# Kernel tuning notes

Measured on AMD Instinct MI355X. Metric: run time of the kernel, lower is better.

The kernel has to match this reference:

```python
import jax, jax.numpy as jnp
import numpy as np
import math

B, S, H, NH = 8, 1024, 768, 12
DH = H // NH  # 64
EPS = 1e-5


def layernorm(x, gamma, beta):
    mu = jnp.mean(x, axis=-1, keepdims=True)
    var = jnp.mean(jnp.square(x - mu), axis=-1, keepdims=True)
    return (x - mu) * jax.lax.rsqrt(var + EPS) * gamma + beta


def setup_inputs() -> dict:
    key = jax.random.key(0)
    ks = jax.random.split(key, 12)
    sc = 1.0 / math.sqrt(H)
    return {
        "x1": jax.random.normal(ks[0], (B, S, H), jnp.float32),
        "weight_mask": jax.random.uniform(ks[1], (B, 1, S, S), jnp.float32),
        "Wq": jax.random.normal(ks[2], (H, H), jnp.float32) * sc,
        "bq": jnp.zeros((H,), jnp.float32),
        "Wk": jax.random.normal(ks[3], (H, H), jnp.float32) * sc,
        "bk": jnp.zeros((H,), jnp.float32),
        "Wv": jax.random.normal(ks[4], (H, H), jnp.float32) * sc,
        "bv": jnp.zeros((H,), jnp.float32),
        "g1": jnp.ones((H,), jnp.float32),
        "be1": jnp.zeros((H,), jnp.float32),
        "g2": jnp.ones((H,), jnp.float32),
        "be2": jnp.zeros((H,), jnp.float32),
        "W1": jax.random.normal(ks[5], (H, 2 * H), jnp.float32) * sc,
        "b1": jnp.zeros((2 * H,), jnp.float32),
        "W2": jax.random.normal(ks[6], (2 * H, H), jnp.float32) * (1.0 / math.sqrt(2 * H)),
        "b2": jnp.zeros((H,), jnp.float32),
    }


def reference(x1, weight_mask, Wq, bq, Wk, bk, Wv, bv, g1, be1, g2, be2, W1, b1, W2, b2):
    # QKV projections [B,S,H]
    q_mixed = x1 @ Wq + bq
    k_mixed = x1 @ Wk + bk
    v_mixed = x1 @ Wv + bv

    def heads(t):  # [B,S,H] -> [B,NH,S,DH]
        return t.reshape(B, S, NH, DH).transpose(0, 2, 1, 3)

    q, k, v = heads(q_mixed), heads(k_mixed), heads(v_mixed)
    scores = jnp.einsum("bhqd,bhkd->bhqk", q, k) / math.sqrt(DH)
    probs = jax.nn.softmax(scores, axis=-1)
    probs = probs * weight_mask  # post-softmax elementwise mask
    ctx = jnp.einsum("bhqk,bhkd->bhqd", probs, v)
    ctx = ctx.transpose(0, 2, 1, 3).reshape(B, S, H)

    # residual uses the mixed query (as in the original code); dropout = eval identity
    x = layernorm(ctx + q_mixed, g1, be1)
    ff = jnp.maximum(x @ W1 + b1, 0.0) @ W2 + b2
    out = layernorm(x + ff, g2, be2)
    return out
```

## Files before the change

kernel.cpp:

```cpp
#include <hip/hip_runtime.h>
#include <math.h>

#define Bsz 8
#define Sq  1024
#define Hd  768
#define NHd 12
#define DHd 64
#define QS  2304

typedef __attribute__((ext_vector_type(8))) short bf16x8;
typedef __attribute__((ext_vector_type(4))) short bf16x4;
typedef __attribute__((ext_vector_type(4))) float f32x4;
typedef __attribute__((ext_vector_type(16))) float f32x16;

__device__ __forceinline__ ushort f2bf(float f) {
    unsigned u = __float_as_uint(f);
    u += 0x7fffu + ((u >> 16) & 1u);
    return (ushort)(u >> 16);
}
__device__ __forceinline__ float bf2f(ushort u) {
    return __uint_as_float(((unsigned)u) << 16);
}
__device__ __forceinline__ void load_lds16(const ushort* g, ushort* l) {
    __builtin_amdgcn_global_load_lds((const __attribute__((address_space(1))) void*)g,
                                     (__attribute__((address_space(3))) void*)l, 16, 0, 0);
}
__device__ __forceinline__ float fexp2(float x) {
#if __has_builtin(__builtin_amdgcn_exp2f)
    return __builtin_amdgcn_exp2f(x);
#else
    return exp2f(x);
#endif
}
__device__ __forceinline__ unsigned pkbf(float a, float b) {
#if __has_builtin(__builtin_amdgcn_perm)
    return __builtin_amdgcn_perm(__float_as_uint(b), __float_as_uint(a), 0x07060302u);
#else
    return (__float_as_uint(a) >> 16) | (__float_as_uint(b) & 0xffff0000u);
#endif
}

__device__ __forceinline__ f32x16 mfma32x8(bf16x4 a, bf16x4 b, f32x16 c) {
#if __has_builtin(__builtin_amdgcn_mfma_f32_32x32x8bf16_1k)
    return __builtin_amdgcn_mfma_f32_32x32x8bf16_1k(a, b, c, 0, 0, 0);
#elif __has_builtin(__builtin_amdgcn_mfma_f32_32x32x8_bf16)
    return __builtin_amdgcn_mfma_f32_32x32x8_bf16(a, b, c, 0, 0, 0);
#else
    bf16x8 a8 = {a[0], a[1], a[2], a[3], 0, 0, 0, 0};
    bf16x8 b8 = {b[0], b[1], b[2], b[3], 0, 0, 0, 0};
    return __builtin_amdgcn_mfma_f32_32x32x16_bf16(a8, b8, c, 0, 0, 0);
#endif
}

#define KSCALE 0.18033688f

__global__ __launch_bounds__(256) void prep(const float* __restrict__ x1,
                                            const float* __restrict__ wmask,
                                            const float* __restrict__ Wq,
                                            const float* __restrict__ Wk,
                                            const float* __restrict__ Wv,
                                            const float* __restrict__ W1,
                                            const float* __restrict__ W2,
                                            const float* __restrict__ bq,
                                            const float* __restrict__ bk,
                                            const float* __restrict__ bv,
                                            ushort* __restrict__ xb,
                                            ushort* __restrict__ maskb,
                                            ushort* __restrict__ WqkvT,
                                            ushort* __restrict__ W1T,
                                            ushort* __restrict__ W2T,
                                            float* __restrict__ qkvbias) {
    const int blk = blockIdx.x;
    const int t   = threadIdx.x;
    __shared__ float tl[32][33];

    if (blk < 4032) {
        const float* in; ushort* out; int Kd, Nd, ntx, tile; float sc;
        if (blk < 1728) {
            const int w = blk / 576; tile = blk % 576;
            in  = (w == 0) ? Wq : (w == 1) ? Wk : Wv;
            out = WqkvT + (size_t)w * 768 * 768;
            Kd = 768; Nd = 768; ntx = 24;
            sc = (w == 1) ? KSCALE : 1.0f;
        } else if (blk < 2880) {
            tile = blk - 1728; in = W1; out = W1T; Kd = 768; Nd = 1536; ntx = 48; sc = 1.0f;
        } else {
            tile = blk - 2880; in = W2; out = W2T; Kd = 1536; Nd = 768; ntx = 24; sc = 1.0f;
        }
        const int n0 = (tile % ntx) * 32, k0 = (tile / ntx) * 32;
        const int tx = t & 31, ty = t >> 5;
#pragma unroll
        for (int i = ty; i < 32; i += 8)
            tl[i][tx] = in[(size_t)(k0 + i) * Nd + n0 + tx] * sc;
        __syncthreads();
#pragma unroll
        for (int i = ty; i < 32; i += 8)
            out[(size_t)(n0 + i) * Kd + k0 + tx] = f2bf(tl[tx][i]);
    } else if (blk < 7616) {
        const int cb = blk - 4032;
        const float4* s4;
        ushort4* d4;
        if (cb < 1536) { s4 = (const float4*)x1    + (size_t)cb * 1024;           d4 = (ushort4*)xb    + (size_t)cb * 1024; }
        else           { s4 = (const float4*)wmask + (size_t)(cb - 1536) * 1024;  d4 = (ushort4*)maskb + (size_t)(cb - 1536) * 1024; }
#pragma unroll
        for (int i = t; i < 1024; i += 256) {
            const float4 f = s4[i];
            ushort4 u;
            u.x = f2bf(f.x); u.y = f2bf(f.y); u.z = f2bf(f.z); u.w = f2bf(f.w);
            d4[i] = u;
        }
    } else {
        for (int i = t; i < 2304; i += 256)
            qkvbias[i] = i < 768 ? bq[i] : (i < 1536 ? bk[i - 768] * KSCALE : bv[i - 1536]);
    }
}

template<int TM, bool RELU, bool OUT_BF16, bool WRITE_VT>
__global__ __launch_bounds__(256) void gemm_mfma(const ushort* __restrict__ A,
                                                 const ushort* __restrict__ BT,
                                                 const float* __restrict__ bias,
                                                 void* __restrict__ Cout,
                                                 ushort* __restrict__ vT,
                                                 int M, int N, int K) {
    const int bm = blockIdx.y * (TM * 32);
    const int bn = blockIdx.x * 128;
    const int t  = threadIdx.x;
    const int wave = t >> 6, lane = t & 63;
    const int l15 = lane & 15, quad = lane >> 4;
    const int wm = (wave >> 1) * (TM * 16), wn = (wave & 1) * 64;

    __shared__ ushort As[TM * 32 * 64];
    __shared__ ushort Bs[128 * 64];

    f32x4 acc[TM][4];
#pragma unroll
    for (int i = 0; i < TM; ++i)
#pragma unroll
        for (int j = 0; j < 4; ++j) acc[i][j] = (f32x4){0, 0, 0, 0};

    const int g_pc = t & 7;

    for (int k0 = 0; k0 < K; k0 += 64) {
#pragma unroll
        for (int it = 0; it < TM; ++it) {
            const int row = (it * 256 + t) >> 3;
            const int cb  = g_pc ^ (row & 7);
            load_lds16(A + (size_t)(bm + row) * K + k0 + cb * 8,
                       As + (size_t)(it * 256 + wave * 64) * 8);
        }
#pragma unroll
        for (int it = 0; it < 4; ++it) {
            const int row = (it * 256 + t) >> 3;
            const int cb  = g_pc ^ (row & 7);
            load_lds16(BT + (size_t)(bn + row) * K + k0 + cb * 8,
                       Bs + (size_t)(it * 256 + wave * 64) * 8);
        }
        __syncthreads();
#pragma unroll
        for (int kk = 0; kk < 64; kk += 32) {
            bf16x8 af[TM], bfr[4];
            const int cbk = (kk >> 3) + quad;
#pragma unroll
            for (int i = 0; i < TM; ++i) {
                const int rowA = wm + i * 16 + l15;
                af[i] = *(const bf16x8*)(As + (size_t)(rowA * 8 + (cbk ^ (rowA & 7))) * 8);
            }
#pragma unroll
            for (int j = 0; j < 4; ++j) {
                const int rowB = wn + j * 16 + l15;
                bfr[j] = *(const bf16x8*)(Bs + (size_t)(rowB * 8 + (cbk ^ (rowB & 7))) * 8);
            }
#pragma unroll
            for (int i = 0; i < TM; ++i)
#pragma unroll
                for (int j = 0; j < 4; ++j)
                    acc[i][j] = __builtin_amdgcn_mfma_f32_16x16x32_bf16(af[i], bfr[j], acc[i][j], 0, 0, 0);
        }
        __syncthreads();
    }

    const bool vblk = WRITE_VT && (bn >= 1536);
#pragma unroll
    for (int i = 0; i < TM; ++i) {
        const int m0 = bm + wm + i * 16 + quad * 4;
#pragma unroll
        for (int j = 0; j < 4; ++j) {
            const int n = bn + wn + j * 16 + l15;
            float v4[4];
#pragma unroll
            for (int r = 0; r < 4; ++r) {
                float v = acc[i][j][r] + bias[n];
                if (RELU) v = fmaxf(v, 0.0f);
                v4[r] = v;
            }
            if (vblk) {
                const int d = n - 1536;
                const int b = m0 >> 10, s = m0 & 1023;
                ushort4 pk;
                pk.x = f2bf(v4[0]); pk.y = f2bf(v4[1]); pk.z = f2bf(v4[2]); pk.w = f2bf(v4[3]);
                *(ushort4*)(vT + ((size_t)(b * NHd + (d >> 6)) * 64 + (d & 63)) * Sq + s) = pk;
            } else {
#pragma unroll
                for (int r = 0; r < 4; ++r) {
                    if (OUT_BF16) ((ushort*)Cout)[(size_t)(m0 + r) * N + n] = f2bf(v4[r]);
                    else          ((float*)Cout)[(size_t)(m0 + r) * N + n] = v4[r];
                }
            }
        }
    }
}

__global__ __launch_bounds__(256, 3) void attn_mfma(const ushort* __restrict__ qkv,
                                                    const ushort* __restrict__ vT,
                                                    const ushort* __restrict__ maskb,
                                                    float* __restrict__ ctx) {
    const int nqt = Sq / 128;
    const int bh  = blockIdx.x / nqt;
    const int qt  = blockIdx.x % nqt;
    const int b   = bh / NHd;
    const int h   = bh % NHd;
    const int t   = threadIdx.x;
    const int wave = t >> 6, lane = t & 63;
    const int l31 = lane & 31, H = lane >> 5;

    __shared__ ushort Ks[2 * 4096];
    __shared__ ushort Vs[2 * 4096];

    const size_t rowbase = (size_t)b * Sq;
    const int q0 = qt * 128 + wave * 32;

    bf16x8 qf[4];
    {
        const ushort* qrow = qkv + (rowbase + q0 + l31) * QS + h * DHd + H * 8;
#pragma unroll
        for (int ds = 0; ds < 4; ++ds) qf[ds] = *(const bf16x8*)(qrow + ds * 16);
    }

    int koff[2][4], voff[2][8];
#pragma unroll
    for (int s = 0; s < 2; ++s) {
#pragma unroll
        for (int ds = 0; ds < 4; ++ds)
            koff[s][ds] = ((s * 32 + l31) * 8 + ((H + 2 * ds) ^ (l31 & 7))) * 8;
#pragma unroll
        for (int ks = 0; ks < 8; ++ks)
            voff[s][ks] = ((s * 32 + l31) * 8 + (ks ^ (l31 & 7))) * 8 + H * 4;
    }

    const int s_pc = t & 7;
    const ushort* kptr[2];
    const ushort* vptr[2];
    int sdst[2];
#pragma unroll
    for (int it = 0; it < 2; ++it) {
        const int row  = (it * 256 + t) >> 3;
        const int gcol = s_pc ^ (row & 7);
        kptr[it] = qkv + (rowbase + row) * QS + Hd + h * DHd + gcol * 8;
        vptr[it] = vT + ((size_t)bh * 64 + row) * Sq + gcol * 8;
        sdst[it] = (it * 256 + t) * 8;
    }
    const ushort* mptr = maskb + ((size_t)b * Sq + q0 + l31) * Sq + H * 4;

#pragma unroll
    for (int it = 0; it < 2; ++it) {
        load_lds16(kptr[it], Ks + sdst[it]);  kptr[it] += 64 * QS;
        load_lds16(vptr[it], Vs + sdst[it]);  vptr[it] += 64;
    }
    __syncthreads();

    f32x16 o0, o1;
#pragma unroll
    for (int r = 0; r < 16; ++r) { o0[r] = 0.0f; o1[r] = 0.0f; }
    float rsum = 0.0f;

    for (int kt = 0; kt < 16; ++kt) {
        const int cur = kt & 1;
        ushort* ksb = Ks + cur * 4096;
        ushort* vsb = Vs + cur * 4096;

        if (kt < 15) {
            ushort* kd = Ks + (cur ^ 1) * 4096;
            ushort* vd = Vs + (cur ^ 1) * 4096;
#pragma unroll
            for (int it = 0; it < 2; ++it) {
                load_lds16(kptr[it], kd + sdst[it]);  kptr[it] += 64 * QS;
                load_lds16(vptr[it], vd + sdst[it]);  vptr[it] += 64;
            }
        }

        ushort4 mv[8];
#pragma unroll
        for (int i = 0; i < 8; ++i) mv[i] = *(const ushort4*)(mptr + i * 8);
        mptr += 64;

        f32x16 s0, s1;
#pragma unroll
        for (int r = 0; r < 16; ++r) { s0[r] = 0.0f; s1[r] = 0.0f; }
#pragma unroll
        for (int ds = 0; ds < 4; ++ds) {
            bf16x8 ka = *(const bf16x8*)(ksb + koff[0][ds]);
            bf16x8 kb = *(const bf16x8*)(ksb + koff[1][ds]);
            s0 = __builtin_amdgcn_mfma_f32_32x32x16_bf16(ka, qf[ds], s0, 0, 0, 0);
            s1 = __builtin_amdgcn_mfma_f32_32x32x16_bf16(kb, qf[ds], s1, 0, 0, 0);
        }

        bf16x4 pf[8];
#pragma unroll
        for (int rr = 0; rr < 4; ++rr) {
            float e0[4], e1[4];
#pragma unroll
            for (int j = 0; j < 4; ++j) {
                e0[j] = fexp2(s0[4 * rr + j]);
                e1[j] = fexp2(s1[4 * rr + j]);
                rsum += e0[j] + e1[j];
            }
            union { uint2 u; bf16x4 v; } p0, p1;
            p0.u.x = pkbf(e0[0] * bf2f(mv[rr].x),     e0[1] * bf2f(mv[rr].y));
            p0.u.y = pkbf(e0[2] * bf2f(mv[rr].z),     e0[3] * bf2f(mv[rr].w));
            p1.u.x = pkbf(e1[0] * bf2f(mv[4 + rr].x), e1[1] * bf2f(mv[4 + rr].y));
            p1.u.y = pkbf(e1[2] * bf2f(mv[4 + rr].z), e1[3] * bf2f(mv[4 + rr].w));
            pf[rr]     = p0.v;
            pf[4 + rr] = p1.v;
        }

#pragma unroll
        for (int ks = 0; ks < 8; ++ks) {
            bf16x4 va = *(const bf16x4*)(vsb + voff[0][ks]);
            bf16x4 vb = *(const bf16x4*)(vsb + voff[1][ks]);
            o0 = mfma32x8(pf[ks], va, o0);
            o1 = mfma32x8(pf[ks], vb, o1);
        }
        __syncthreads();
    }

    rsum += __shfl_xor(rsum, 32);

#pragma unroll
    for (int r = 0; r < 16; ++r) {
        const int ql  = (r & 3) + 8 * (r >> 2) + 4 * H;
        const float inv = 1.0f / __shfl(rsum, ql);
        const size_t row = rowbase + q0 + ql;
        ctx[row * Hd + h * DHd + l31]      = o0[r] * inv;
        ctx[row * Hd + h * DHd + 32 + l31] = o1[r] * inv;
    }
}

template<bool RES_BF16, bool EMIT_BF16, bool EMIT_F32>
__global__ __launch_bounds__(256) void ln_fused(const float* __restrict__ a,
                                                const void* __restrict__ res, int res_stride,
                                                const float* __restrict__ g,
                                                const float* __restrict__ be,
                                                float* __restrict__ outf,
                                                ushort* __restrict__ outb) {
    const int row = blockIdx.x;
    const int t   = threadIdx.x;
    const float* pa = a + (size_t)row * Hd;
    __shared__ float red[4];
    float v[3];
#pragma unroll
    for (int i = 0; i < 3; ++i) {
        const int idx = t + i * 256;
        float rv;
        if (RES_BF16) rv = bf2f(((const ushort*)res)[(size_t)row * res_stride + idx]);
        else          rv = ((const float*)res)[(size_t)row * res_stride + idx];
        v[i] = pa[idx] + rv;
    }

    float s = v[0] + v[1] + v[2];
#pragma unroll
    for (int off = 32; off > 0; off >>= 1) s += __shfl_xor(s, off);
    if ((t & 63) == 0) red[t >> 6] = s;
    __syncthreads();
    const float mu = (red[0] + red[1] + red[2] + red[3]) * (1.0f / Hd);
    __syncthreads();

    float sq = 0.0f;
#pragma unroll
    for (int i = 0; i < 3; ++i) {
        v[i] -= mu;
        sq = fmaf(v[i], v[i], sq);
    }
#pragma unroll
    for (int off = 32; off > 0; off >>= 1) sq += __shfl_xor(sq, off);
    if ((t & 63) == 0) red[t >> 6] = sq;
    __syncthreads();
    const float var = (red[0] + red[1] + red[2] + red[3]) * (1.0f / Hd);
    const float rsq = rsqrtf(var + 1e-5f);
#pragma unroll
    for (int i = 0; i < 3; ++i) {
        const int idx = t + i * 256;
        const float o = v[i] * rsq * g[idx] + be[idx];
        if (EMIT_F32)  outf[(size_t)row * Hd + idx] = o;
        if (EMIT_BF16) outb[(size_t)row * Hd + idx] = f2bf(o);
    }
}

extern "C" void kernel_launch(void* const* d_in, const int* in_sizes, int n_in,
                              void* d_out, int out_size, void* d_ws, size_t ws_size,
                              hipStream_t stream) {
    const float* x1    = (const float*)d_in[0];
    const float* wmask = (const float*)d_in[1];
    const float* Wq    = (const float*)d_in[2];
    const float* bq    = (const float*)d_in[3];
    const float* Wk    = (const float*)d_in[4];
    const float* bk    = (const float*)d_in[5];
    const float* Wv    = (const float*)d_in[6];
    const float* bv    = (const float*)d_in[7];
    const float* g1    = (const float*)d_in[8];
    const float* be1   = (const float*)d_in[9];
    const float* g2    = (const float*)d_in[10];
    const float* be2   = (const float*)d_in[11];
    const float* W1    = (const float*)d_in[12];
    const float* b1    = (const float*)d_in[13];
    const float* W2    = (const float*)d_in[14];
    const float* b2    = (const float*)d_in[15];
    float* out = (float*)d_out;

    const size_t NT = (size_t)Bsz * Sq * Hd;
    const size_t NM = (size_t)Bsz * Sq * Sq;
    const int M = Bsz * Sq;

    char* p = (char*)d_ws;
    ushort* xb     = (ushort*)p;  p += NT * 2;
    ushort* WqkvT  = (ushort*)p;  p += (size_t)2304 * 768 * 2;
    ushort* W1T    = (ushort*)p;  p += (size_t)1536 * 768 * 2;
    ushort* W2T    = (ushort*)p;  p += (size_t)768 * 1536 * 2;
    float*  qkvbias= (float*)p;   p += 2304 * 4 + 256;
    ushort* qkvb   = (ushort*)p;  p += (size_t)M * QS * 2;
    ushort* maskb  = (ushort*)p;  p += NM * 2;
    ushort* vT     = (ushort*)p;  p += (size_t)Bsz * NHd * DHd * Sq * 2;
    float*  ctxb   = (float*)p;   p += NT * 4;
    ushort* xbf    = (ushort*)p;  p += NT * 2;
    ushort* hb     = qkvb;
    float*  ffb    = ctxb;

    dim3 blk(256);

    prep<<<dim3(7617), blk, 0, stream>>>(x1, wmask, Wq, Wk, Wv, W1, W2, bq, bk, bv,
                                         xb, maskb, WqkvT, W1T, W2T, qkvbias);

    gemm_mfma<4, false, true, true><<<dim3(2304 / 128, M / 128), blk, 0, stream>>>(
        xb, WqkvT, qkvbias, qkvb, vT, M, 2304, 768);

    attn_mfma<<<dim3(Bsz * NHd * (Sq / 128)), blk, 0, stream>>>(qkvb, vT, maskb, ctxb);

    ln_fused<true, true, false><<<dim3(M), blk, 0, stream>>>(ctxb, qkvb, QS, g1, be1, nullptr, xbf);

    gemm_mfma<4, true, true, false><<<dim3(1536 / 128, M / 128), blk, 0, stream>>>(
        xbf, W1T, b1, hb, nullptr, M, 1536, 768);

    gemm_mfma<2, false, false, false><<<dim3(768 / 128, M / 64), blk, 0, stream>>>(
        hb, W2T, b2, ffb, nullptr, M, 768, 1536);

    ln_fused<true, false, true><<<dim3(M), blk, 0, stream>>>(ffb, xbf, Hd, g2, be2, out, nullptr);
}
```

Before: 345.0 us.

## Stage mask tiles through double-buffered LDS with async global-to-LDS loads

```diff
diff --git a/kernel.cpp b/kernel.cpp
--- a/kernel.cpp
+++ b/kernel.cpp
@@ -210,7 +210,7 @@
     }
 }
 
-__global__ __launch_bounds__(256, 3) void attn_mfma(const ushort* __restrict__ qkv,
+__global__ __launch_bounds__(256, 2) void attn_mfma(const ushort* __restrict__ qkv,
                                                     const ushort* __restrict__ vT,
                                                     const ushort* __restrict__ maskb,
                                                     float* __restrict__ ctx) {
@@ -225,6 +225,7 @@
 
     __shared__ ushort Ks[2 * 4096];
     __shared__ ushort Vs[2 * 4096];
+    __shared__ ushort Ms[2 * 8192];
 
     const size_t rowbase = (size_t)b * Sq;
     const int q0 = qt * 128 + wave * 32;
@@ -236,7 +237,7 @@
         for (int ds = 0; ds < 4; ++ds) qf[ds] = *(const bf16x8*)(qrow + ds * 16);
     }
 
-    int koff[2][4], voff[2][8];
+    int koff[2][4], voff[2][8], moff[8];
 #pragma unroll
     for (int s = 0; s < 2; ++s) {
 #pragma unroll
@@ -245,12 +246,19 @@
 #pragma unroll
         for (int ks = 0; ks < 8; ++ks)
             voff[s][ks] = ((s * 32 + l31) * 8 + (ks ^ (l31 & 7))) * 8 + H * 4;
+    }
+    {
+        const int qrow = wave * 32 + l31;
+#pragma unroll
+        for (int ks = 0; ks < 8; ++ks)
+            moff[ks] = (qrow * 8 + (ks ^ (l31 & 7))) * 8 + H * 4;
     }
 
     const int s_pc = t & 7;
     const ushort* kptr[2];
     const ushort* vptr[2];
-    int sdst[2];
+    const ushort* mptr[4];
+    int sdst[2], mdst[4];
 #pragma unroll
     for (int it = 0; it < 2; ++it) {
         const int row  = (it * 256 + t) >> 3;
@@ -259,12 +267,22 @@
         vptr[it] = vT + ((size_t)bh * 64 + row) * Sq + gcol * 8;
         sdst[it] = (it * 256 + t) * 8;
     }
-    const ushort* mptr = maskb + ((size_t)b * Sq + q0 + l31) * Sq + H * 4;
+#pragma unroll
+    for (int it = 0; it < 4; ++it) {
+        const int row  = (it * 256 + t) >> 3;
+        const int gcol = s_pc ^ (row & 7);
+        mptr[it] = maskb + ((size_t)b * Sq + qt * 128 + row) * Sq + gcol * 8;
+        mdst[it] = (it * 256 + t) * 8;
+    }
 
 #pragma unroll
     for (int it = 0; it < 2; ++it) {
         load_lds16(kptr[it], Ks + sdst[it]);  kptr[it] += 64 * QS;
         load_lds16(vptr[it], Vs + sdst[it]);  vptr[it] += 64;
+    }
+#pragma unroll
+    for (int it = 0; it < 4; ++it) {
+        load_lds16(mptr[it], Ms + mdst[it]);  mptr[it] += 64;
     }
     __syncthreads();
 
@@ -277,21 +295,22 @@
         const int cur = kt & 1;
         ushort* ksb = Ks + cur * 4096;
         ushort* vsb = Vs + cur * 4096;
+        ushort* msb = Ms + cur * 8192;
 
         if (kt < 15) {
             ushort* kd = Ks + (cur ^ 1) * 4096;
             ushort* vd = Vs + (cur ^ 1) * 4096;
+            ushort* md = Ms + (cur ^ 1) * 8192;
 #pragma unroll
             for (int it = 0; it < 2; ++it) {
                 load_lds16(kptr[it], kd + sdst[it]);  kptr[it] += 64 * QS;
                 load_lds16(vptr[it], vd + sdst[it]);  vptr[it] += 64;
             }
-        }
-
-        ushort4 mv[8];
-#pragma unroll
-        for (int i = 0; i < 8; ++i) mv[i] = *(const ushort4*)(mptr + i * 8);
-        mptr += 64;
+#pragma unroll
+            for (int it = 0; it < 4; ++it) {
+                load_lds16(mptr[it], md + mdst[it]);  mptr[it] += 64;
+            }
+        }
 
         f32x16 s0, s1;
 #pragma unroll
@@ -303,6 +322,10 @@
             s0 = __builtin_amdgcn_mfma_f32_32x32x16_bf16(ka, qf[ds], s0, 0, 0, 0);
             s1 = __builtin_amdgcn_mfma_f32_32x32x16_bf16(kb, qf[ds], s1, 0, 0, 0);
         }
+
+        ushort4 mv[8];
+#pragma unroll
+        for (int ks = 0; ks < 8; ++ks) mv[ks] = *(const ushort4*)(msb + moff[ks]);
 
         bf16x4 pf[8];
 #pragma unroll
```

Result: no change. 345.7 us (+0.2%).
